# Kernel optimization log

Hardware: AMD Instinct MI355X
Metric: run time of the kernel (lower is better)

## Reference

```python
import jax, jax.numpy as jnp
import numpy as np

DIM = 768
HIDDEN = 4 * DIM          # shared expert hidden
NUM_EXPERTS = 8
TOPK = 2
D_LOW = DIM // 4          # 192


def setup_inputs() -> dict:
    key = jax.random.key(0)
    ks = jax.random.split(key, 8)
    B, C, H, W = 8, DIM, 32, 32
    x = jax.random.normal(ks[0], (B, C, H, W), dtype=jnp.float32)
    # shared expert (1x1 convs == per-pixel linear)
    w1 = jax.random.normal(ks[1], (HIDDEN, DIM), dtype=jnp.float32) * 0.02
    b1 = jnp.zeros((HIDDEN,), dtype=jnp.float32)
    w2 = jax.random.normal(ks[2], (DIM, HIDDEN), dtype=jnp.float32) * 0.02
    b2 = jnp.zeros((DIM,), dtype=jnp.float32)
    # router params (torch Linear weight layout [out, in])
    w_down = jax.random.normal(ks[3], (NUM_EXPERTS * D_LOW, DIM), dtype=jnp.float32) * 0.02
    router_w = jax.random.normal(ks[4], (1, D_LOW), dtype=jnp.float32) * 0.02
    w_up = jax.random.normal(ks[5], (NUM_EXPERTS, D_LOW, DIM), dtype=jnp.float32) * 0.02
    return {"x": x, "w1": w1, "b1": b1, "w2": w2, "b2": b2,
            "w_down": w_down, "router_w": router_w, "w_up": w_up}


def _gelu(v):
    # torch nn.GELU default = exact erf variant
    return jax.nn.gelu(v, approximate=False)


def reference(x, w1, b1, w2, b2, w_down, router_w, w_up):
    B, C, H, W = x.shape
    # ---- shared expert: conv1x1 -> GELU -> conv1x1 ----
    h = jnp.einsum('bchw,oc->bohw', x, w1) + b1[None, :, None, None]
    shared = jnp.einsum('bohw,co->bchw', _gelu(h), w2) + b2[None, :, None, None]
    # ---- AoE router over tokens ----
    N = H * W
    x_flat = x.reshape(B, C, N).transpose(0, 2, 1).reshape(B * N, C)  # [T, C]
    feats = (x_flat @ w_down.T).reshape(-1, NUM_EXPERTS, D_LOW)       # [T, E, d_low]
    logits = jnp.einsum('ted,d->te', feats, router_w[0])              # [T, E]
    probs = jax.nn.softmax(logits, axis=-1)
    topk_w, topk_i = jax.lax.top_k(probs, TOPK)                       # [T, k]
    topk_w = topk_w / jnp.sum(topk_w, axis=-1, keepdims=True)
    sel = jnp.take_along_axis(feats, topk_i[:, :, None], axis=1)      # [T, k, d_low]
    act = _gelu(sel)
    sel_w_up = w_up[topk_i]                                           # [T, k, d_low, C]
    expert_out = jnp.einsum('tkd,tkdm->tkm', act, sel_w_up)           # [T, k, C]
    weighted = jnp.sum(expert_out * topk_w[:, :, None], axis=1)       # [T, C]
    # aux load-balance loss
    mean_prob = jnp.mean(probs, axis=0)
    one_hot = jnp.sum(jax.nn.one_hot(topk_i, NUM_EXPERTS, dtype=probs.dtype), axis=1)
    mean_load = jnp.mean(one_hot, axis=0)
    aux_loss = NUM_EXPERTS * jnp.sum(mean_prob * mean_load)
    aoe = weighted.reshape(B, N, C).transpose(0, 2, 1).reshape(B, C, H, W)
    return x + shared + aoe, aux_loss
```

## Files before the change

kernel.cpp:

```cpp
#include <hip/hip_runtime.h>
#include <cstdint>
#include <cmath>

#define DIM   768
#define HID   3072
#define NEXP  8
#define DLOW  192
#define NPB   1024
#define NTOK  8192
#define KD    1536
#define KCAT  4608

typedef unsigned short ushort_t;
typedef short   short8  __attribute__((ext_vector_type(8)));
typedef float   float4v __attribute__((ext_vector_type(4)));

__device__ inline ushort_t f2b(float f) {
    union { float f; unsigned int i; } v; v.f = f;
    unsigned int x = v.i;
    return (ushort_t)((x + 0x7fffu + ((x >> 16) & 1u)) >> 16);
}
__device__ inline float gelu_fast(float x) {
    const float z = 1.5957691216057308f * x * __builtin_fmaf(0.044715f * x, x, 1.0f);
    return x * __builtin_amdgcn_rcpf(1.0f + __expf(-z));
}

__device__ __forceinline__ void async_ld16(const ushort_t* g, ushort_t* l) {
    __builtin_amdgcn_global_load_lds(
        (const __attribute__((address_space(1))) void*)g,
        (__attribute__((address_space(3))) void*)l,
        16, 0, 0);
}

__global__ __launch_bounds__(512)
void gemm_in(const ushort_t* __restrict__ A, const ushort_t* __restrict__ B,
             ushort_t* __restrict__ Cb, const float* __restrict__ bias,
             const int* __restrict__ tokE, const float* __restrict__ tokW,
             const float* __restrict__ accbuf, float* __restrict__ outAux,
             int m_base)
{
    __shared__ __align__(16) ushort_t As[256 * 64];
    __shared__ __align__(16) ushort_t Bs[128 * 64];

    const int tid  = threadIdx.x;
    const int lane = tid & 63;
    const int wave = tid >> 6;
    const int quad = lane >> 4;
    const int l16  = lane & 15;
    const int wm   = (wave >> 1) * 64;
    const int wn   = (wave & 1) * 64;

    const int nwg = gridDim.x * gridDim.y;
    const int bid = blockIdx.y * gridDim.x + blockIdx.x;
    const int swz = (bid & 7) * (nwg >> 3) + (bid >> 3);
    const int m0  = (swz / gridDim.x) * 256;
    const int n0  = (swz % gridDim.x) * 128;

    float4v acc[4][4];
#pragma unroll
    for (int i = 0; i < 4; i++)
#pragma unroll
        for (int j = 0; j < 4; j++) acc[i][j] = (float4v)0.0f;

    const ushort_t* ga[4]; ushort_t* la[4];
#pragma unroll
    for (int j = 0; j < 4; j++) {
        const int f = j * 512 + tid;
        const int mm = f >> 3;
        const int gs = ((f & 7) ^ (mm & 7)) * 8;
        ga[j] = A + (size_t)(m0 + mm) * DIM + gs;
        la[j] = &As[f * 8];
    }
    const ushort_t* gb[2]; ushort_t* lb[2];
#pragma unroll
    for (int j = 0; j < 2; j++) {
        const int f = j * 512 + tid;
        const int mm = f >> 3;
        const int gs = ((f & 7) ^ (mm & 7)) * 8;
        gb[j] = B + (size_t)(n0 + mm) * DIM + gs;
        lb[j] = &Bs[f * 8];
    }

    const ushort_t* pa[2][4]; const ushort_t* pb[2][4];
#pragma unroll
    for (int kh = 0; kh < 2; kh++)
#pragma unroll
        for (int i = 0; i < 4; i++) {
            const int ra = wm + i * 16 + l16;
            pa[kh][i] = &As[ra * 64 + (((quad + 4 * kh) ^ (ra & 7)) * 8)];
            const int rb = wn + i * 16 + l16;
            pb[kh][i] = &Bs[rb * 64 + (((quad + 4 * kh) ^ (rb & 7)) * 8)];
        }

    for (int k0 = 0; k0 < DIM; k0 += 64) {
        __syncthreads();
#pragma unroll
        for (int j = 0; j < 4; j++) async_ld16(ga[j] + k0, la[j]);
#pragma unroll
        for (int j = 0; j < 2; j++) async_ld16(gb[j] + k0, lb[j]);
        __syncthreads();
#pragma unroll
        for (int kh = 0; kh < 2; kh++) {
            short8 af[4], bv[4];
#pragma unroll
            for (int i = 0; i < 4; i++) af[i] = *(const short8*)pa[kh][i];
#pragma unroll
            for (int i = 0; i < 4; i++) bv[i] = *(const short8*)pb[kh][i];
#pragma unroll
            for (int im = 0; im < 4; im++)
#pragma unroll
                for (int in = 0; in < 4; in++)
                    acc[im][in] = __builtin_amdgcn_mfma_f32_16x16x32_bf16(
                        af[im], bv[in], acc[im][in], 0, 0, 0);
        }
    }

    if (n0 < HID) {
#pragma unroll
        for (int in = 0; in < 4; in++) {
            const int col = n0 + wn + in * 16 + l16;
            const float bvv = bias[col];
#pragma unroll
            for (int im = 0; im < 4; im++) {
                const int rowl = m0 + wm + im * 16 + quad * 4;
#pragma unroll
                for (int r = 0; r < 4; r++)
                    Cb[(size_t)(rowl + r) * KCAT + col] =
                        f2b(gelu_fast(acc[im][in][r] + bvv));
            }
        }
        if (m_base == 0 && blockIdx.x == 0 && blockIdx.y == 0 && tid == 0) {
            float aux = 0.0f;
            for (int e = 0; e < 8; e++) aux += accbuf[e] * accbuf[8 + e];
            outAux[0] = aux * 8.0f / ((float)NTOK * (float)NTOK);
        }
    } else {
        int eidx[4];
#pragma unroll
        for (int in = 0; in < 4; in++)
            eidx[in] = (n0 + wn + in * 16 - HID) / DLOW;
#pragma unroll
        for (int im = 0; im < 4; im++) {
            const int rowl = m0 + wm + im * 16 + quad * 4;
#pragma unroll
            for (int r = 0; r < 4; r++) {
                const int g = m_base + rowl + r;
                const int e0 = tokE[2 * g], e1 = tokE[2 * g + 1];
                const float w0 = tokW[2 * g], w1 = tokW[2 * g + 1];
#pragma unroll
                for (int in = 0; in < 4; in++) {
                    const int col = n0 + wn + in * 16 + l16;
                    const float m = (eidx[in] == e0) ? w0
                                  : ((eidx[in] == e1) ? w1 : 0.0f);
                    Cb[(size_t)(rowl + r) * KCAT + col] =
                        f2b(gelu_fast(acc[im][in][r]) * m);
                }
            }
        }
    }
}

__global__ __launch_bounds__(256, 2)
void gemm_out(const ushort_t* __restrict__ A, const ushort_t* __restrict__ B,
              float* __restrict__ out, const float* __restrict__ bias,
              const float* __restrict__ X, int m_base)
{
    __shared__ __align__(16) ushort_t As[2 * 128 * 64];
    __shared__ __align__(16) ushort_t Bs[2 * 96 * 64];

    const int tid  = threadIdx.x;
    const int lane = tid & 63;
    const int wave = tid >> 6;
    const int quad = lane >> 4;
    const int l16  = lane & 15;
    const int wm   = (wave >> 1) * 64;
    const int wn   = (wave & 1) * 48;

    const int nwg = gridDim.x * gridDim.y;
    const int bid = blockIdx.y * gridDim.x + blockIdx.x;
    const int swz = (bid & 7) * (nwg >> 3) + (bid >> 3);
    const int m0  = (swz / gridDim.x) * 128;
    const int n0  = (swz % gridDim.x) * 96;

    float4v acc[4][3];
#pragma unroll
    for (int i = 0; i < 4; i++)
#pragma unroll
        for (int j = 0; j < 3; j++) acc[i][j] = (float4v)0.0f;

    const ushort_t* ga[4]; ushort_t* la[4];
#pragma unroll
    for (int j = 0; j < 4; j++) {
        const int f = j * 256 + tid;
        const int mm = f >> 3;
        const int gs = ((f & 7) ^ (mm & 7)) * 8;
        ga[j] = A + (size_t)(m0 + mm) * KCAT + gs;
        la[j] = &As[f * 8];
    }
    const ushort_t* gb[3]; ushort_t* lb[3];
#pragma unroll
    for (int j = 0; j < 3; j++) {
        const int f = j * 256 + tid;
        const int mm = f >> 3;
        const int gs = ((f & 7) ^ (mm & 7)) * 8;
        gb[j] = B + (size_t)(n0 + mm) * KCAT + gs;
        lb[j] = &Bs[f * 8];
    }

    const ushort_t* pa[2][4]; const ushort_t* pb[2][3];
#pragma unroll
    for (int kh = 0; kh < 2; kh++) {
#pragma unroll
        for (int i = 0; i < 4; i++) {
            const int ra = wm + i * 16 + l16;
            pa[kh][i] = &As[ra * 64 + (((quad + 4 * kh) ^ (ra & 7)) * 8)];
        }
#pragma unroll
        for (int i = 0; i < 3; i++) {
            const int rb = wn + i * 16 + l16;
            pb[kh][i] = &Bs[rb * 64 + (((quad + 4 * kh) ^ (rb & 7)) * 8)];
        }
    }

    for (int k0 = 0; k0 < KCAT; k0 += 128) {
        __syncthreads();
#pragma unroll
        for (int j = 0; j < 4; j++) async_ld16(ga[j] + k0,      la[j]);
#pragma unroll
        for (int j = 0; j < 4; j++) async_ld16(ga[j] + k0 + 64, la[j] + 128 * 64);
#pragma unroll
        for (int j = 0; j < 3; j++) async_ld16(gb[j] + k0,      lb[j]);
#pragma unroll
        for (int j = 0; j < 3; j++) async_ld16(gb[j] + k0 + 64, lb[j] + 96 * 64);
        __syncthreads();
#pragma unroll
        for (int kp = 0; kp < 2; kp++) {
            const int ao = kp * 128 * 64, bo = kp * 96 * 64;
#pragma unroll
            for (int kh = 0; kh < 2; kh++) {
                short8 af[4], bv[3];
#pragma unroll
                for (int i = 0; i < 4; i++) af[i] = *(const short8*)(pa[kh][i] + ao);
#pragma unroll
                for (int i = 0; i < 3; i++) bv[i] = *(const short8*)(pb[kh][i] + bo);
#pragma unroll
                for (int im = 0; im < 4; im++)
#pragma unroll
                    for (int in = 0; in < 3; in++)
                        acc[im][in] = __builtin_amdgcn_mfma_f32_16x16x32_bf16(
                            af[im], bv[in], acc[im][in], 0, 0, 0);
            }
        }
    }

#pragma unroll
    for (int in = 0; in < 3; in++) {
        const int col = n0 + wn + in * 16 + l16;
        const float bvv = bias[col];
#pragma unroll
        for (int im = 0; im < 4; im++) {
            const int grow = m_base + m0 + wm + im * 16 + quad * 4;
            const int bb = grow >> 10, nn = grow & 1023;
            const size_t base = ((size_t)bb * DIM + col) * NPB + nn;
            const float4 xv = *(const float4*)(X + base);
            float4 v;
            v.x = acc[im][in][0] + bvv + xv.x;
            v.y = acc[im][in][1] + bvv + xv.y;
            v.z = acc[im][in][2] + bvv + xv.z;
            v.w = acc[im][in][3] + bvv + xv.w;
            *(float4*)(out + base) = v;
        }
    }
}

#define NB_TX   1536
#define NB_WUP  1152
#define NB_W2   (DIM * HID / 4 / 256)
#define NB_WIN  (KCAT * DIM / 4 / 256)
#define NB_WEFF (NEXP * DIM / 256)
#define NB_PREP (NB_TX + NB_WUP + NB_W2 + NB_WIN + NB_WEFF)

__global__ __launch_bounds__(256)
void prep_all(const float* __restrict__ x,  ushort_t* __restrict__ XT,
              const float* __restrict__ wup, ushort_t* __restrict__ Wcat,
              const float* __restrict__ w2,  const float* __restrict__ w1,
              const float* __restrict__ wdn, ushort_t* __restrict__ Win,
              const float* __restrict__ rw,  float* __restrict__ Weff,
              float* __restrict__ accb)
{
    __shared__ ushort_t tile[32][33];
    __shared__ __align__(16) ushort_t t2[64 * 68];
    const int tid = threadIdx.x;
    const int tx = tid & 31, ty = tid >> 5;
    int blk = blockIdx.x;

    if (blk < NB_TX) {
        const int bx = blk & 15;
        const int rest = blk >> 4;
        const int by = rest % 12, b = rest / 12;
        const int n0 = bx * 64, c0 = by * 64;
#pragma unroll
        for (int j = 0; j < 4; j++) {
            const int idx = j * 256 + tid;
            const int c = idx >> 4, q = idx & 15;
            const float4 v = *(const float4*)(
                x + ((size_t)b * DIM + c0 + c) * NPB + n0 + 4 * q);
            uint2 p;
            p.x = (unsigned)f2b(v.x) | ((unsigned)f2b(v.y) << 16);
            p.y = (unsigned)f2b(v.z) | ((unsigned)f2b(v.w) << 16);
            *(uint2*)&t2[c * 68 + 4 * q] = p;
        }
        __syncthreads();
#pragma unroll
        for (int j = 0; j < 2; j++) {
            const int w = (tid >> 3) + 32 * j;
            const int p = tid & 7;
            ushort_t u[8];
#pragma unroll
            for (int cc = 0; cc < 8; cc++) u[cc] = t2[(8 * p + cc) * 68 + w];
            uint4 o;
            o.x = (unsigned)u[0] | ((unsigned)u[1] << 16);
            o.y = (unsigned)u[2] | ((unsigned)u[3] << 16);
            o.z = (unsigned)u[4] | ((unsigned)u[5] << 16);
            o.w = (unsigned)u[6] | ((unsigned)u[7] << 16);
            *(uint4*)&XT[((size_t)b * NPB + n0 + w) * DIM + c0 + 8 * p] = o;
        }
        return;
    }
    blk -= NB_TX;
    if (blk < NB_WUP) {
        const int bx = blk % 24, by = blk / 24;
        const int c0 = bx * 32, k0 = by * 32;
#pragma unroll
        for (int j = 0; j < 4; j++)
            tile[ty + 8 * j][tx] =
                f2b(wup[(size_t)(k0 + ty + 8 * j) * DIM + c0 + tx]);
        __syncthreads();
#pragma unroll
        for (int j = 0; j < 4; j++)
            Wcat[(size_t)(c0 + ty + 8 * j) * KCAT + HID + k0 + tx] =
                tile[tx][ty + 8 * j];
        return;
    }
    blk -= NB_WUP;
    if (blk < NB_W2) {
        const int i = blk * 256 + tid;
        const int c = i / (HID / 4), h = (i % (HID / 4)) * 4;
        const float4 v = *(const float4*)(w2 + (size_t)c * HID + h);
        uint2 p;
        p.x = (unsigned)f2b(v.x) | ((unsigned)f2b(v.y) << 16);
        p.y = (unsigned)f2b(v.z) | ((unsigned)f2b(v.w) << 16);
        *(uint2*)(Wcat + (size_t)c * KCAT + h) = p;
        return;
    }
    blk -= NB_W2;
    if (blk < NB_WIN) {
        const int i = blk * 256 + tid;
        const int n1 = HID * DIM / 4;
        const float4 v = (i < n1) ? ((const float4*)w1)[i]
                                  : ((const float4*)wdn)[i - n1];
        uint2 p;
        p.x = (unsigned)f2b(v.x) | ((unsigned)f2b(v.y) << 16);
        p.y = (unsigned)f2b(v.z) | ((unsigned)f2b(v.w) << 16);
        ((uint2*)Win)[i] = p;
        return;
    }
    blk -= NB_WIN;
    {
        const int idx = blk * 256 + tid;
        const int e = idx / DIM, c = idx % DIM;
        float s = 0.0f;
        for (int d = 0; d < DLOW; d++)
            s += wdn[(size_t)(e * DLOW + d) * DIM + c] * rw[d];
        Weff[idx] = s;
        if (blk == 0 && tid < 16) accb[tid] = 0.0f;
    }
}

__global__ __launch_bounds__(256)
void router_kernel(const float* __restrict__ x, const float* __restrict__ Weff,
                   int* __restrict__ tokE, float* __restrict__ tokW,
                   float* __restrict__ accbuf)
{
    __shared__ float sW[NEXP * DIM];
    __shared__ float sAcc[16];
    const int tid = threadIdx.x;
    for (int i = tid; i < NEXP * DIM; i += 256) sW[i] = Weff[i];
    if (tid < 16) sAcc[tid] = 0.0f;
    __syncthreads();

    const int t = blockIdx.x * 256 + tid;
    const int b = t >> 10, n = t & 1023;
    const float* xb = x + (size_t)b * DIM * NPB + n;

    float lg[8];
#pragma unroll
    for (int e = 0; e < 8; e++) lg[e] = 0.0f;
#pragma unroll 8
    for (int c = 0; c < DIM; c++) {
        const float xv = xb[(size_t)c * NPB];
#pragma unroll
        for (int e = 0; e < 8; e++) lg[e] += xv * sW[e * DIM + c];
    }

    float mx = lg[0];
#pragma unroll
    for (int e = 1; e < 8; e++) mx = fmaxf(mx, lg[e]);
    float pr[8], s = 0.0f;
#pragma unroll
    for (int e = 0; e < 8; e++) { pr[e] = expf(lg[e] - mx); s += pr[e]; }
    const float inv = 1.0f / s;
#pragma unroll
    for (int e = 0; e < 8; e++) pr[e] *= inv;
    int e0 = 0;
#pragma unroll
    for (int e = 1; e < 8; e++) if (pr[e] > pr[e0]) e0 = e;
    int e1 = (e0 == 0) ? 1 : 0;
#pragma unroll
    for (int e = 0; e < 8; e++) if (e != e0 && pr[e] > pr[e1]) e1 = e;
    const float wsum = pr[e0] + pr[e1];
    tokE[2 * t + 0] = e0;  tokE[2 * t + 1] = e1;
    tokW[2 * t + 0] = pr[e0] / wsum;  tokW[2 * t + 1] = pr[e1] / wsum;

#pragma unroll
    for (int e = 0; e < 8; e++) atomicAdd(&sAcc[e], pr[e]);
    atomicAdd(&sAcc[8 + e0], 1.0f);
    atomicAdd(&sAcc[8 + e1], 1.0f);
    __syncthreads();
    if (tid < 16) atomicAdd(&accbuf[tid], sAcc[tid]);
}

extern "C" void kernel_launch(void* const* d_in, const int* in_sizes, int n_in,
                              void* d_out, int out_size, void* d_ws, size_t ws_size,
                              hipStream_t stream)
{
    (void)in_sizes; (void)n_in; (void)out_size;

    const float* x   = (const float*)d_in[0];
    const float* w1  = (const float*)d_in[1];
    const float* b1  = (const float*)d_in[2];
    const float* w2  = (const float*)d_in[3];
    const float* b2  = (const float*)d_in[4];
    const float* wdn = (const float*)d_in[5];
    const float* rw  = (const float*)d_in[6];
    const float* wup = (const float*)d_in[7];
    float* out = (float*)d_out;

    char* ws = (char*)d_ws;
    size_t off = 0;
    ushort_t* XTbf = (ushort_t*)(ws + off); off += (size_t)NTOK * DIM * 2;
    ushort_t* Win  = (ushort_t*)(ws + off); off += (size_t)KCAT * DIM * 2;
    ushort_t* Wcat = (ushort_t*)(ws + off); off += (size_t)DIM * KCAT * 2;
    float*    Weff = (float*)  (ws + off);  off += (size_t)NEXP * DIM * 4;
    int*      tokE = (int*)    (ws + off);  off += (size_t)NTOK * 2 * 4;
    float*    tokW = (float*)  (ws + off);  off += (size_t)NTOK * 2 * 4;
    float*    accb = (float*)  (ws + off);  off += 256;

    int chunk = NTOK / 4;
    if      (ws_size >= off + (size_t)NTOK * KCAT * 2)       chunk = NTOK;
    else if (ws_size >= off + (size_t)(NTOK / 2) * KCAT * 2) chunk = NTOK / 2;
    ushort_t* HU = (ushort_t*)(ws + off);

    prep_all<<<NB_PREP, 256, 0, stream>>>(x, XTbf, wup, Wcat, w2, w1, wdn,
                                          Win, rw, Weff, accb);
    router_kernel<<<NTOK / 256, 256, 0, stream>>>(x, Weff, tokE, tokW, accb);

    for (int c = 0; c < NTOK / chunk; c++) {
        const ushort_t* Ax = XTbf + (size_t)c * chunk * DIM;
        const int m_base = c * chunk;
        gemm_in<<<dim3(KCAT / 128, chunk / 256), 512, 0, stream>>>(
            Ax, Win, HU, b1, tokE, tokW, accb, out + (size_t)NTOK * DIM, m_base);
        gemm_out<<<dim3(DIM / 96, chunk / 128), 256, 0, stream>>>(
            HU, Wcat, out, b2, x, m_base);
    }
}
```

Measured before the change: 307.3 us.

## Double-buffer LDS tiles with prefetch-two pipelining in both GEMMs

Both GEMM main loops become a two-stage LDS ping-pong. Global-to-LDS async loads for tile t+2 are issued right after the fragments of tile t are read into registers, and explicit vmcnt waits, barriers and setprio are used so that memory latency overlaps the MFMA work. gemm_in also shrinks from a 256x128 tile with 512 threads to a 128x128 tile with 256 threads, with launch bounds allowing two blocks per CU to raise occupancy. The hand-tuned waitcnt counts and the removal of the __syncthreads pairs could be fragile if the compiler reorders loads, and the smaller M tile lowers data reuse per block.

```diff
diff --git a/kernel.cpp b/kernel.cpp
--- a/kernel.cpp
+++ b/kernel.cpp
@@ -32,15 +32,16 @@
         16, 0, 0);
 }
 
-__global__ __launch_bounds__(512)
+
+__global__ __launch_bounds__(256, 2)
 void gemm_in(const ushort_t* __restrict__ A, const ushort_t* __restrict__ B,
              ushort_t* __restrict__ Cb, const float* __restrict__ bias,
              const int* __restrict__ tokE, const float* __restrict__ tokW,
              const float* __restrict__ accbuf, float* __restrict__ outAux,
              int m_base)
 {
-    __shared__ __align__(16) ushort_t As[256 * 64];
-    __shared__ __align__(16) ushort_t Bs[128 * 64];
+    __shared__ __align__(16) ushort_t As[2 * 128 * 64];
+    __shared__ __align__(16) ushort_t Bs[2 * 128 * 64];
 
     const int tid  = threadIdx.x;
     const int lane = tid & 63;
@@ -53,7 +54,7 @@
     const int nwg = gridDim.x * gridDim.y;
     const int bid = blockIdx.y * gridDim.x + blockIdx.x;
     const int swz = (bid & 7) * (nwg >> 3) + (bid >> 3);
-    const int m0  = (swz / gridDim.x) * 256;
+    const int m0  = (swz / gridDim.x) * 128;
     const int n0  = (swz % gridDim.x) * 128;
 
     float4v acc[4][4];
@@ -65,16 +66,16 @@
     const ushort_t* ga[4]; ushort_t* la[4];
 #pragma unroll
     for (int j = 0; j < 4; j++) {
-        const int f = j * 512 + tid;
+        const int f = j * 256 + tid;
         const int mm = f >> 3;
         const int gs = ((f & 7) ^ (mm & 7)) * 8;
         ga[j] = A + (size_t)(m0 + mm) * DIM + gs;
         la[j] = &As[f * 8];
     }
-    const ushort_t* gb[2]; ushort_t* lb[2];
-#pragma unroll
-    for (int j = 0; j < 2; j++) {
-        const int f = j * 512 + tid;
+    const ushort_t* gb[4]; ushort_t* lb[4];
+#pragma unroll
+    for (int j = 0; j < 4; j++) {
+        const int f = j * 256 + tid;
         const int mm = f >> 3;
         const int gs = ((f & 7) ^ (mm & 7)) * 8;
         gb[j] = B + (size_t)(n0 + mm) * DIM + gs;
@@ -92,28 +93,60 @@
             pb[kh][i] = &Bs[rb * 64 + (((quad + 4 * kh) ^ (rb & 7)) * 8)];
         }
 
-    for (int k0 = 0; k0 < DIM; k0 += 64) {
-        __syncthreads();
-#pragma unroll
-        for (int j = 0; j < 4; j++) async_ld16(ga[j] + k0, la[j]);
-#pragma unroll
-        for (int j = 0; j < 2; j++) async_ld16(gb[j] + k0, lb[j]);
-        __syncthreads();
-#pragma unroll
-        for (int kh = 0; kh < 2; kh++) {
-            short8 af[4], bv[4];
-#pragma unroll
-            for (int i = 0; i < 4; i++) af[i] = *(const short8*)pa[kh][i];
-#pragma unroll
-            for (int i = 0; i < 4; i++) bv[i] = *(const short8*)pb[kh][i];
-#pragma unroll
-            for (int im = 0; im < 4; im++)
-#pragma unroll
-                for (int in = 0; in < 4; in++)
-                    acc[im][in] = __builtin_amdgcn_mfma_f32_16x16x32_bf16(
-                        af[im], bv[in], acc[im][in], 0, 0, 0);
-        }
-    }
+#define STG_I(k0, ao, bo) do {                                              \
+    _Pragma("unroll")                                                       \
+    for (int j = 0; j < 4; j++) async_ld16(ga[j] + (k0), la[j] + (ao));     \
+    _Pragma("unroll")                                                       \
+    for (int j = 0; j < 4; j++) async_ld16(gb[j] + (k0), lb[j] + (bo)); } while (0)
+
+#define BODY_I(t, ao, bo) do {                                              \
+    short8 af0[4], bv0[4], af1[4], bv1[4];                                  \
+    _Pragma("unroll")                                                       \
+    for (int i = 0; i < 4; i++) {                                           \
+        af0[i] = *(const short8*)(pa[0][i] + (ao));                         \
+        af1[i] = *(const short8*)(pa[1][i] + (ao));                         \
+        bv0[i] = *(const short8*)(pb[0][i] + (bo));                         \
+        bv1[i] = *(const short8*)(pb[1][i] + (bo));                         \
+    }                                                                       \
+    asm volatile("s_waitcnt lgkmcnt(0)" ::: "memory");                      \
+    __builtin_amdgcn_sched_barrier(0);                                      \
+    __builtin_amdgcn_s_barrier();           \
+    __builtin_amdgcn_sched_barrier(0);          \
+    const bool st_ = (t) + 2 < 12;                                          \
+    if (st_) STG_I(((t) + 2) * 64, ao, bo);                                 \
+    __builtin_amdgcn_s_setprio(1);                                          \
+    _Pragma("unroll")                                                       \
+    for (int im = 0; im < 4; im++)                                          \
+        _Pragma("unroll")                                                   \
+        for (int in = 0; in < 4; in++)                                      \
+            acc[im][in] = __builtin_amdgcn_mfma_f32_16x16x32_bf16(          \
+                af0[im], bv0[in], acc[im][in], 0, 0, 0);                    \
+    _Pragma("unroll")                                                       \
+    for (int im = 0; im < 4; im++)                                          \
+        _Pragma("unroll")                                                   \
+        for (int in = 0; in < 4; in++)                                      \
+            acc[im][in] = __builtin_amdgcn_mfma_f32_16x16x32_bf16(          \
+                af1[im], bv1[in], acc[im][in], 0, 0, 0);                    \
+    __builtin_amdgcn_s_setprio(0);                                          \
+    if (st_) asm volatile("s_waitcnt vmcnt(8)" ::: "memory");               \
+    else     asm volatile("s_waitcnt vmcnt(0)" ::: "memory");               \
+    __builtin_amdgcn_sched_barrier(0);                                      \
+    __builtin_amdgcn_s_barrier();             \
+    __builtin_amdgcn_sched_barrier(0);                                      \
+} while (0)
+
+    STG_I(0, 0, 0);
+    STG_I(64, 128 * 64, 128 * 64);
+    asm volatile("s_waitcnt vmcnt(8)" ::: "memory");
+    __builtin_amdgcn_s_barrier();
+    __builtin_amdgcn_sched_barrier(0);
+
+    for (int tt = 0; tt < 12; tt += 2) {
+        BODY_I(tt, 0, 0);
+        BODY_I(tt + 1, 128 * 64, 128 * 64);
+    }
+#undef STG_I
+#undef BODY_I
 
     if (n0 < HID) {
 #pragma unroll
@@ -222,36 +255,63 @@
         }
     }
 
-    for (int k0 = 0; k0 < KCAT; k0 += 128) {
-        __syncthreads();
-#pragma unroll
-        for (int j = 0; j < 4; j++) async_ld16(ga[j] + k0,      la[j]);
-#pragma unroll
-        for (int j = 0; j < 4; j++) async_ld16(ga[j] + k0 + 64, la[j] + 128 * 64);
-#pragma unroll
-        for (int j = 0; j < 3; j++) async_ld16(gb[j] + k0,      lb[j]);
-#pragma unroll
-        for (int j = 0; j < 3; j++) async_ld16(gb[j] + k0 + 64, lb[j] + 96 * 64);
-        __syncthreads();
-#pragma unroll
-        for (int kp = 0; kp < 2; kp++) {
-            const int ao = kp * 128 * 64, bo = kp * 96 * 64;
-#pragma unroll
-            for (int kh = 0; kh < 2; kh++) {
-                short8 af[4], bv[3];
-#pragma unroll
-                for (int i = 0; i < 4; i++) af[i] = *(const short8*)(pa[kh][i] + ao);
-#pragma unroll
-                for (int i = 0; i < 3; i++) bv[i] = *(const short8*)(pb[kh][i] + bo);
-#pragma unroll
-                for (int im = 0; im < 4; im++)
-#pragma unroll
-                    for (int in = 0; in < 3; in++)
-                        acc[im][in] = __builtin_amdgcn_mfma_f32_16x16x32_bf16(
-                            af[im], bv[in], acc[im][in], 0, 0, 0);
-            }
-        }
-    }
+#define STG_O(k0, ao, bo) do {                                              \
+    _Pragma("unroll")                                                       \
+    for (int j = 0; j < 4; j++) async_ld16(ga[j] + (k0), la[j] + (ao));     \
+    _Pragma("unroll")                                                       \
+    for (int j = 0; j < 3; j++) async_ld16(gb[j] + (k0), lb[j] + (bo)); } while (0)
+
+#define BODY_O(t, ao, bo) do {                                              \
+    short8 af0[4], bv0[3], af1[4], bv1[3];                                  \
+    _Pragma("unroll")                                                       \
+    for (int i = 0; i < 4; i++) {                                           \
+        af0[i] = *(const short8*)(pa[0][i] + (ao));                         \
+        af1[i] = *(const short8*)(pa[1][i] + (ao));                         \
+    }                                                                       \
+    _Pragma("unroll")                                                       \
+    for (int i = 0; i < 3; i++) {                                           \
+        bv0[i] = *(const short8*)(pb[0][i] + (bo));                         \
+        bv1[i] = *(const short8*)(pb[1][i] + (bo));                         \
+    }                                                                       \
+    asm volatile("s_waitcnt lgkmcnt(0)" ::: "memory");                      \
+    __builtin_amdgcn_sched_barrier(0);                                      \
+    __builtin_amdgcn_s_barrier();           \
+    __builtin_amdgcn_sched_barrier(0);          \
+    const bool st_ = (t) + 2 < 72;                                          \
+    if (st_) STG_O(((t) + 2) * 64, ao, bo);                                 \
+    __builtin_amdgcn_s_setprio(1);                                          \
+    _Pragma("unroll")                                                       \
+    for (int im = 0; im < 4; im++)                                          \
+        _Pragma("unroll")                                                   \
+        for (int in = 0; in < 3; in++)                                      \
+            acc[im][in] = __builtin_amdgcn_mfma_f32_16x16x32_bf16(          \
+                af0[im], bv0[in], acc[im][in], 0, 0, 0);                    \
+    _Pragma("unroll")                                                       \
+    for (int im = 0; im < 4; im++)                                          \
+        _Pragma("unroll")                                                   \
+        for (int in = 0; in < 3; in++)                                      \
+            acc[im][in] = __builtin_amdgcn_mfma_f32_16x16x32_bf16(          \
+                af1[im], bv1[in], acc[im][in], 0, 0, 0);                    \
+    __builtin_amdgcn_s_setprio(0);                                          \
+    if (st_) asm volatile("s_waitcnt vmcnt(7)" ::: "memory");               \
+    else     asm volatile("s_waitcnt vmcnt(0)" ::: "memory");               \
+    __builtin_amdgcn_sched_barrier(0);                                      \
+    __builtin_amdgcn_s_barrier();             \
+    __builtin_amdgcn_sched_barrier(0);                                      \
+} while (0)
+
+    STG_O(0, 0, 0);
+    STG_O(64, 128 * 64, 96 * 64);
+    asm volatile("s_waitcnt vmcnt(7)" ::: "memory");
+    __builtin_amdgcn_s_barrier();
+    __builtin_amdgcn_sched_barrier(0);
+
+    for (int tt = 0; tt < 72; tt += 2) {
+        BODY_O(tt, 0, 0);
+        BODY_O(tt + 1, 128 * 64, 96 * 64);
+    }
+#undef STG_O
+#undef BODY_O
 
 #pragma unroll
     for (int in = 0; in < 3; in++) {
@@ -468,7 +528,7 @@
     for (int c = 0; c < NTOK / chunk; c++) {
         const ushort_t* Ax = XTbf + (size_t)c * chunk * DIM;
         const int m_base = c * chunk;
-        gemm_in<<<dim3(KCAT / 128, chunk / 256), 512, 0, stream>>>(
+        gemm_in<<<dim3(KCAT / 128, chunk / 128), 256, 0, stream>>>(
             Ax, Win, HU, b1, tokE, tokW, accb, out + (size_t)NTOK * DIM, m_base);
         gemm_out<<<dim3(DIM / 96, chunk / 128), 256, 0, stream>>>(
             HU, Wcat, out, b2, x, m_base);
```

Result: slower. 313.8 us (+2.1%).
